# Kernel optimization log

Hardware: AMD Instinct MI355X
Metric: run time of the kernel (lower is better)

The kernel has to match this reference:

```python
import jax, jax.numpy as jnp
import numpy as np

B, S = 4096, 256
D = 32  # output_size // 4


def setup_inputs() -> dict:
    key = jax.random.key(0)
    ks = jax.random.split(key, 32)
    # continuous features
    cont_p = jax.random.normal(ks[0], (B, S, 3), dtype=jnp.float32)
    cont_c = jax.random.normal(ks[1], (B, S, 2), dtype=jnp.float32)
    # categorical features, per-column vocab sizes from Embedding tables
    vocabs_p = [2, 2, 2, 11, 34]
    cat_p = jnp.stack([
        jax.random.randint(ks[2 + i], (B, S), 0, v, dtype=jnp.int32)
        for i, v in enumerate(vocabs_p)], axis=2)
    vocabs_c = [19, 31]
    cat_c = jnp.stack([
        jax.random.randint(ks[7 + i], (B, S), 0, v, dtype=jnp.int32)
        for i, v in enumerate(vocabs_c)], axis=2)
    lengths = jax.random.randint(ks[9], (B,), 1, S + 1, dtype=jnp.int32)

    def lin(k, fan_in, fan_out):
        bound = 1.0 / np.sqrt(fan_in)
        kw, kb = jax.random.split(k)
        w = jax.random.uniform(kw, (fan_in, fan_out), jnp.float32, -bound, bound)
        b = jax.random.uniform(kb, (fan_out,), jnp.float32, -bound, bound)
        return w, b

    w_p1, b_p1 = lin(ks[10], 3, D)
    w_p2, b_p2 = lin(ks[11], D, D)
    w_c1, b_c1 = lin(ks[12], 2, D)
    w_c2, b_c2 = lin(ks[13], D, D)
    emb_gender = jax.random.normal(ks[14], (2, D), dtype=jnp.float32)
    emb_korean = jax.random.normal(ks[15], (2, D), dtype=jnp.float32)
    emb_primary = jax.random.normal(ks[16], (2, D), dtype=jnp.float32)
    emb_job = jax.random.normal(ks[17], (11, D), dtype=jnp.float32)
    emb_rep = jax.random.normal(ks[18], (34, D), dtype=jnp.float32)
    emb_place = jax.random.normal(ks[19], (19, D), dtype=jnp.float32)
    emb_add = jax.random.normal(ks[20], (31, D), dtype=jnp.float32)
    w_fc1, b_fc1 = lin(ks[21], 128, 64)
    w_fc2, b_fc2 = lin(ks[22], 64, 2)

    return dict(cont_p=cont_p, cont_c=cont_c, cat_p=cat_p, cat_c=cat_c,
                lengths=lengths,
                w_p1=w_p1, b_p1=b_p1, w_p2=w_p2, b_p2=b_p2,
                w_c1=w_c1, b_c1=b_c1, w_c2=w_c2, b_c2=b_c2,
                emb_gender=emb_gender, emb_korean=emb_korean,
                emb_primary=emb_primary, emb_job=emb_job, emb_rep=emb_rep,
                emb_place=emb_place, emb_add=emb_add,
                w_fc1=w_fc1, b_fc1=b_fc1, w_fc2=w_fc2, b_fc2=b_fc2)


def reference(cont_p, cont_c, cat_p, cat_c, lengths,
              w_p1, b_p1, w_p2, b_p2, w_c1, b_c1, w_c2, b_c2,
              emb_gender, emb_korean, emb_primary, emb_job, emb_rep,
              emb_place, emb_add, w_fc1, b_fc1, w_fc2, b_fc2):
    # small per-token MLPs on continuous features -> [B,S,D]
    hp = jax.nn.relu(cont_p @ w_p1 + b_p1) @ w_p2 + b_p2
    hc = jax.nn.relu(cont_c @ w_c1 + b_c1) @ w_c2 + b_c2
    # multi-table embedding lookups, averaged per group -> [B,S,D]
    ep = (emb_gender[cat_p[:, :, 0]] + emb_korean[cat_p[:, :, 1]] +
          emb_primary[cat_p[:, :, 2]] + emb_job[cat_p[:, :, 3]] +
          emb_rep[cat_p[:, :, 4]]) / 5.0
    ec = (emb_place[cat_c[:, :, 0]] + emb_add[cat_c[:, :, 1]]) / 2.0
    # concat order matches torch: (cat_p, cat_c, cont_p, cont_c) -> [B,S,128]
    x = jnp.concatenate([ep, ec, hp, hc], axis=2)
    # ragged mean pool over first lengths[i] positions (masked segment mean)
    mask = (jnp.arange(x.shape[1])[None, :] < lengths[:, None])
    pooled = jnp.sum(x * mask[:, :, None], axis=1) / lengths[:, None].astype(x.dtype)
    # head: relu(fc1) -> relu(fc2); dropout p=0.0 is identity
    h = jax.nn.relu(pooled @ w_fc1 + b_fc1)
    return jax.nn.relu(h @ w_fc2 + b_fc2)
```

## Files before the change

kernel.cpp:

```cpp
#include <hip/hip_runtime.h>


#define BDIM 64

__global__ __launch_bounds__(BDIM)
void mlpreg_kernel(const float* __restrict__ cont_p,
                   const float* __restrict__ cont_c,
                   const int* __restrict__ cat_p,
                   const int* __restrict__ cat_c,
                   const int* __restrict__ lengths,
                   const float* __restrict__ w_p1, const float* __restrict__ b_p1,
                   const float* __restrict__ w_p2, const float* __restrict__ b_p2,
                   const float* __restrict__ w_c1, const float* __restrict__ b_c1,
                   const float* __restrict__ w_c2, const float* __restrict__ b_c2,
                   const float* __restrict__ emb_g,  const float* __restrict__ emb_k,
                   const float* __restrict__ emb_pr, const float* __restrict__ emb_j,
                   const float* __restrict__ emb_r,  const float* __restrict__ emb_pl,
                   const float* __restrict__ emb_a,
                   const float* __restrict__ w_fc1, const float* __restrict__ b_fc1,
                   const float* __restrict__ w_fc2, const float* __restrict__ b_fc2,
                   float* __restrict__ out)
{
    constexpr int S = 256;
    __shared__ float sP4[S * 4];
    __shared__ float sC2[S * 2];
    __shared__ int   hist[96];
    __shared__ float sPacc[64];
    __shared__ float sPooled[128];

    const int lane = threadIdx.x;
    const int b    = blockIdx.x;
    int L = lengths[b];
    if (L < 1) L = 1;
    if (L > S) L = S;
    const float invL = 1.0f / (float)L;
    const float Lf   = (float)L;

    const int*   kp = cat_p  + (size_t)b * (S * 5);
    const int*   kc = cat_c  + (size_t)b * (S * 2);
    const float* gp = cont_p + (size_t)b * (S * 3);
    const float* gc = cont_c + (size_t)b * (S * 2);

    hist[lane] = 0;
    if (lane < 32) hist[64 + lane] = 0;
    __syncthreads();

    for (int t = lane; t < L; t += BDIM) {
        float c0 = gp[t * 3 + 0], c1 = gp[t * 3 + 1], c2 = gp[t * 3 + 2];
        float4 v; v.x = c0; v.y = c1; v.z = c2; v.w = 0.f;
        *(float4*)&sP4[t * 4] = v;
        float2 u = *(const float2*)(gc + t * 2);
        *(float2*)&sC2[t * 2] = u;
    }

    int sg = 0, sk = 0, spr = 0;
    for (int i = lane; i < 5 * L; i += BDIM) {
        int v = kp[i];
        int col = i % 5;
        if      (col == 0) sg  += v;
        else if (col == 1) sk  += v;
        else if (col == 2) spr += v;
        else if (col == 3) atomicAdd(&hist[v], 1);
        else               atomicAdd(&hist[11 + v], 1);
    }
    for (int i = lane; i < 2 * L; i += BDIM) {
        int v = kc[i];
        atomicAdd(&hist[(i & 1) ? (64 + v) : (45 + v)], 1);
    }
    #pragma unroll
    for (int d = 32; d; d >>= 1) {
        sg  += __shfl_xor(sg,  d);
        sk  += __shfl_xor(sk,  d);
        spr += __shfl_xor(spr, d);
    }
    __syncthreads();

    const int pr = lane >> 5, ch = lane & 31;
    const float wp0 = w_p1[ch], wp1 = w_p1[32 + ch], wp2 = w_p1[64 + ch], bp = b_p1[ch];
    const float wc0 = w_c1[ch], wc1 = w_c1[32 + ch], bc = b_c1[ch];

    float accP = 0.f, accC = 0.f;
    #pragma unroll 4
    for (int t = pr; t < L; t += 2) {
        float4 cp = *(const float4*)&sP4[t * 4];
        float2 cc = *(const float2*)&sC2[t * 2];
        accP += fmaxf(fmaf(cp.x, wp0, fmaf(cp.y, wp1, fmaf(cp.z, wp2, bp))), 0.f);
        accC += fmaxf(fmaf(cc.x, wc0, fmaf(cc.y, wc1, bc)), 0.f);
    }
    accP += __shfl_down(accP, 32);
    accC += __shfl_down(accC, 32);
    if (lane < 32) {
        sPacc[ch]      = accP * invL;
        sPacc[32 + ch] = accC * invL;
    }

    if (pr == 0) {
        float cg = (float)sg, ck = (float)sk, cp = (float)spr;
        float s0 = fmaf(Lf - cg, emb_g[ch],  fmaf(cg, emb_g[32 + ch],
                   fmaf(Lf - ck, emb_k[ch],  ck * emb_k[32 + ch])));
        float s1 = fmaf(Lf - cp, emb_pr[ch], cp * emb_pr[32 + ch]);
        #pragma unroll
        for (int r = 0; r < 11; ++r) s0 = fmaf((float)hist[r],      emb_j[r * 32 + ch], s0);
        #pragma unroll
        for (int r = 0; r < 34; r += 2) {
            s0 = fmaf((float)hist[11 + r],     emb_r[(r + 0) * 32 + ch], s0);
            s1 = fmaf((float)hist[11 + r + 1], emb_r[(r + 1) * 32 + ch], s1);
        }
        sPooled[ch] = (s0 + s1) * (invL * 0.2f);
    } else {
        float s0 = 0.f, s1 = 0.f;
        #pragma unroll
        for (int r = 0; r < 19; ++r) s0 = fmaf((float)hist[45 + r], emb_pl[r * 32 + ch], s0);
        #pragma unroll
        for (int r = 0; r < 31; r += 2) {
            s0 = fmaf((float)hist[64 + r], emb_a[(r + 0) * 32 + ch], s0);
            if (r + 1 < 31)
                s1 = fmaf((float)hist[64 + r + 1], emb_a[(r + 1) * 32 + ch], s1);
        }
        sPooled[32 + ch] = (s0 + s1) * (invL * 0.5f);
    }
    __syncthreads();

    if (pr == 0) {
        float v0 = b_p2[ch], v1 = 0.f;
        #pragma unroll
        for (int k = 0; k < 32; k += 2) {
            v0 = fmaf(sPacc[k],     w_p2[(k + 0) * 32 + ch], v0);
            v1 = fmaf(sPacc[k + 1], w_p2[(k + 1) * 32 + ch], v1);
        }
        sPooled[64 + ch] = v0 + v1;
    } else {
        float v0 = b_c2[ch], v1 = 0.f;
        #pragma unroll
        for (int k = 0; k < 32; k += 2) {
            v0 = fmaf(sPacc[32 + k],     w_c2[(k + 0) * 32 + ch], v0);
            v1 = fmaf(sPacc[32 + k + 1], w_c2[(k + 1) * 32 + ch], v1);
        }
        sPooled[96 + ch] = v0 + v1;
    }
    __syncthreads();

    const float* wk = w_fc1 + lane;
    float v0 = b_fc1[lane], v1 = 0.f, v2 = 0.f, v3 = 0.f;
    #pragma unroll 8
    for (int k = 0; k < 128; k += 4) {
        float4 x = *(const float4*)&sPooled[k];
        v0 = fmaf(x.x, wk[(size_t)(k + 0) * 64], v0);
        v1 = fmaf(x.y, wk[(size_t)(k + 1) * 64], v1);
        v2 = fmaf(x.z, wk[(size_t)(k + 2) * 64], v2);
        v3 = fmaf(x.w, wk[(size_t)(k + 3) * 64], v3);
    }
    float h = fmaxf((v0 + v1) + (v2 + v3), 0.f);

    float p0 = h * w_fc2[lane * 2 + 0];
    float p1 = h * w_fc2[lane * 2 + 1];
    #pragma unroll
    for (int d = 32; d; d >>= 1) {
        p0 += __shfl_xor(p0, d);
        p1 += __shfl_xor(p1, d);
    }
    if (lane == 0) {
        float2 o;
        o.x = fmaxf(p0 + b_fc2[0], 0.f);
        o.y = fmaxf(p1 + b_fc2[1], 0.f);
        *(float2*)&out[(size_t)b * 2] = o;
    }
}

extern "C" void kernel_launch(void* const* d_in, const int* in_sizes, int n_in,
                              void* d_out, int out_size, void* d_ws, size_t ws_size,
                              hipStream_t stream) {
    const float* cont_p = (const float*)d_in[0];
    const float* cont_c = (const float*)d_in[1];
    const int*   cat_p  = (const int*)d_in[2];
    const int*   cat_c  = (const int*)d_in[3];
    const int*   lens   = (const int*)d_in[4];
    const float* w_p1   = (const float*)d_in[5];
    const float* b_p1   = (const float*)d_in[6];
    const float* w_p2   = (const float*)d_in[7];
    const float* b_p2   = (const float*)d_in[8];
    const float* w_c1   = (const float*)d_in[9];
    const float* b_c1   = (const float*)d_in[10];
    const float* w_c2   = (const float*)d_in[11];
    const float* b_c2   = (const float*)d_in[12];
    const float* emb_g  = (const float*)d_in[13];
    const float* emb_k  = (const float*)d_in[14];
    const float* emb_pr = (const float*)d_in[15];
    const float* emb_j  = (const float*)d_in[16];
    const float* emb_r  = (const float*)d_in[17];
    const float* emb_pl = (const float*)d_in[18];
    const float* emb_a  = (const float*)d_in[19];
    const float* w_fc1  = (const float*)d_in[20];
    const float* b_fc1  = (const float*)d_in[21];
    const float* w_fc2  = (const float*)d_in[22];
    const float* b_fc2  = (const float*)d_in[23];
    float* out = (float*)d_out;

    const int B = 4096;
    hipLaunchKernelGGL(mlpreg_kernel, dim3(B), dim3(BDIM), 0, stream,
                       cont_p, cont_c, cat_p, cat_c, lens,
                       w_p1, b_p1, w_p2, b_p2, w_c1, b_c1, w_c2, b_c2,
                       emb_g, emb_k, emb_pr, emb_j, emb_r, emb_pl, emb_a,
                       w_fc1, b_fc1, w_fc2, b_fc2, out);
}
```

Baseline: 144.9 us.

## Widen per-row block to 256 threads and split all phases across four waves

Raises the block from one wave to four waves per batch row. All row inputs are loaded up front into registers with coalesced flat indexing before the shared-memory writes, so each thread has many loads in flight. The token MLP, embedding histogram dot products, second-layer MLPs and fc1 are then partitioned across waves, with cross-wave reductions through shared memory. This aims to hide global load latency and shorten the serial per-row chain, at the cost of more barriers and more threads idle in the later small phases.

```diff
diff --git a/kernel.cpp b/kernel.cpp
--- a/kernel.cpp
+++ b/kernel.cpp
@@ -1,9 +1,9 @@
 #include <hip/hip_runtime.h>
 
 
-#define BDIM 64
-
-__global__ __launch_bounds__(BDIM)
+#define BDIM 256
+
+__global__ __launch_bounds__(BDIM, 8)
 void mlpreg_kernel(const float* __restrict__ cont_p,
                    const float* __restrict__ cont_c,
                    const int* __restrict__ cat_p,
@@ -22,14 +22,17 @@
                    float* __restrict__ out)
 {
     constexpr int S = 256;
-    __shared__ float sP4[S * 4];
-    __shared__ float sC2[S * 2];
+    __shared__ float sContP[S * 3];
+    __shared__ float sContC[S * 2];
     __shared__ int   hist[96];
+    __shared__ int   sBin[4][3];
+    __shared__ float sRedP[128], sRedC[128];
     __shared__ float sPacc[64];
     __shared__ float sPooled[128];
-
-    const int lane = threadIdx.x;
-    const int b    = blockIdx.x;
+    __shared__ float sRedF[BDIM];
+
+    const int tid = threadIdx.x;
+    const int b   = blockIdx.x;
     int L = lengths[b];
     if (L < 1) L = 1;
     if (L > S) L = S;
@@ -41,129 +44,167 @@
     const float* gp = cont_p + (size_t)b * (S * 3);
     const float* gc = cont_c + (size_t)b * (S * 2);
 
-    hist[lane] = 0;
-    if (lane < 32) hist[64 + lane] = 0;
-    __syncthreads();
-
-    for (int t = lane; t < L; t += BDIM) {
-        float c0 = gp[t * 3 + 0], c1 = gp[t * 3 + 1], c2 = gp[t * 3 + 2];
-        float4 v; v.x = c0; v.y = c1; v.z = c2; v.w = 0.f;
-        *(float4*)&sP4[t * 4] = v;
-        float2 u = *(const float2*)(gc + t * 2);
-        *(float2*)&sC2[t * 2] = u;
-    }
+    const int n3 = 3 * L, n2 = 2 * L, n5 = 5 * L;
+    float rp0 = (tid       < n3) ? gp[tid]       : 0.f;
+    float rp1 = (tid + 256 < n3) ? gp[tid + 256] : 0.f;
+    float rp2 = (tid + 512 < n3) ? gp[tid + 512] : 0.f;
+    float rc0 = (tid       < n2) ? gc[tid]       : 0.f;
+    float rc1 = (tid + 256 < n2) ? gc[tid + 256] : 0.f;
+    int rk[5];
+    #pragma unroll
+    for (int j = 0; j < 5; ++j) {
+        int ii = tid + 256 * j;
+        rk[j] = (ii < n5) ? kp[ii] : -1;
+    }
+    int rq0 = (tid       < n2) ? kc[tid]       : -1;
+    int rq1 = (tid + 256 < n2) ? kc[tid + 256] : -1;
+
+    if (tid < 96) hist[tid] = 0;
+    __syncthreads();
+
+    if (tid       < n3) sContP[tid]       = rp0;
+    if (tid + 256 < n3) sContP[tid + 256] = rp1;
+    if (tid + 512 < n3) sContP[tid + 512] = rp2;
+    if (tid       < n2) sContC[tid]       = rc0;
+    if (tid + 256 < n2) sContC[tid + 256] = rc1;
 
     int sg = 0, sk = 0, spr = 0;
-    for (int i = lane; i < 5 * L; i += BDIM) {
-        int v = kp[i];
-        int col = i % 5;
-        if      (col == 0) sg  += v;
-        else if (col == 1) sk  += v;
-        else if (col == 2) spr += v;
-        else if (col == 3) atomicAdd(&hist[v], 1);
-        else               atomicAdd(&hist[11 + v], 1);
-    }
-    for (int i = lane; i < 2 * L; i += BDIM) {
-        int v = kc[i];
-        atomicAdd(&hist[(i & 1) ? (64 + v) : (45 + v)], 1);
-    }
+    #pragma unroll
+    for (int j = 0; j < 5; ++j) {
+        int ii = tid + 256 * j;
+        if (ii < n5) {
+            int col = ii % 5, v = rk[j];
+            if      (col == 0) sg  += v;
+            else if (col == 1) sk  += v;
+            else if (col == 2) spr += v;
+            else if (col == 3) atomicAdd(&hist[v], 1);
+            else               atomicAdd(&hist[11 + v], 1);
+        }
+    }
+    if (rq0 >= 0) atomicAdd(&hist[((tid & 1) ? 64 : 45) + rq0], 1);
+    if (rq1 >= 0) atomicAdd(&hist[((tid & 1) ? 64 : 45) + rq1], 1);
+
     #pragma unroll
     for (int d = 32; d; d >>= 1) {
         sg  += __shfl_xor(sg,  d);
         sk  += __shfl_xor(sk,  d);
         spr += __shfl_xor(spr, d);
     }
-    __syncthreads();
-
-    const int pr = lane >> 5, ch = lane & 31;
+    const int wv = tid >> 6, lane = tid & 63;
+    if (lane == 0) { sBin[wv][0] = sg; sBin[wv][1] = sk; sBin[wv][2] = spr; }
+    __syncthreads();
+
+    const int g8 = tid >> 5, ch = tid & 31, h = lane >> 5;
     const float wp0 = w_p1[ch], wp1 = w_p1[32 + ch], wp2 = w_p1[64 + ch], bp = b_p1[ch];
     const float wc0 = w_c1[ch], wc1 = w_c1[32 + ch], bc = b_c1[ch];
-
     float accP = 0.f, accC = 0.f;
-    #pragma unroll 4
-    for (int t = pr; t < L; t += 2) {
-        float4 cp = *(const float4*)&sP4[t * 4];
-        float2 cc = *(const float2*)&sC2[t * 2];
-        accP += fmaxf(fmaf(cp.x, wp0, fmaf(cp.y, wp1, fmaf(cp.z, wp2, bp))), 0.f);
-        accC += fmaxf(fmaf(cc.x, wc0, fmaf(cc.y, wc1, bc)), 0.f);
+    #pragma unroll 2
+    for (int t = g8; t < L; t += 8) {
+        float c0 = sContP[3 * t], c1 = sContP[3 * t + 1], c2 = sContP[3 * t + 2];
+        float d0 = sContC[2 * t], d1 = sContC[2 * t + 1];
+        accP += fmaxf(fmaf(c0, wp0, fmaf(c1, wp1, fmaf(c2, wp2, bp))), 0.f);
+        accC += fmaxf(fmaf(d0, wc0, fmaf(d1, wc1, bc)), 0.f);
     }
     accP += __shfl_down(accP, 32);
     accC += __shfl_down(accC, 32);
-    if (lane < 32) {
-        sPacc[ch]      = accP * invL;
-        sPacc[32 + ch] = accC * invL;
-    }
-
-    if (pr == 0) {
-        float cg = (float)sg, ck = (float)sk, cp = (float)spr;
-        float s0 = fmaf(Lf - cg, emb_g[ch],  fmaf(cg, emb_g[32 + ch],
-                   fmaf(Lf - ck, emb_k[ch],  ck * emb_k[32 + ch])));
-        float s1 = fmaf(Lf - cp, emb_pr[ch], cp * emb_pr[32 + ch]);
-        #pragma unroll
-        for (int r = 0; r < 11; ++r) s0 = fmaf((float)hist[r],      emb_j[r * 32 + ch], s0);
-        #pragma unroll
-        for (int r = 0; r < 34; r += 2) {
-            s0 = fmaf((float)hist[11 + r],     emb_r[(r + 0) * 32 + ch], s0);
-            s1 = fmaf((float)hist[11 + r + 1], emb_r[(r + 1) * 32 + ch], s1);
-        }
-        sPooled[ch] = (s0 + s1) * (invL * 0.2f);
+    if (lane < 32) { sRedP[wv * 32 + ch] = accP; sRedC[wv * 32 + ch] = accC; }
+    __syncthreads();
+
+    if (wv == 0) {
+        float sgT  = (float)(sBin[0][0] + sBin[1][0] + sBin[2][0] + sBin[3][0]);
+        float skT  = (float)(sBin[0][1] + sBin[1][1] + sBin[2][1] + sBin[3][1]);
+        float sprT = (float)(sBin[0][2] + sBin[1][2] + sBin[2][2] + sBin[3][2]);
+        float s = 0.f;
+        if (h == 0) {
+            s  = fmaf(Lf - sgT,  emb_g[ch],  sgT  * emb_g[32 + ch]);
+            s += fmaf(Lf - sprT, emb_pr[ch], sprT * emb_pr[32 + ch]);
+            #pragma unroll
+            for (int r = 0; r < 6; ++r)  s = fmaf((float)hist[r],      emb_j[r * 32 + ch], s);
+            #pragma unroll
+            for (int r = 0; r < 17; ++r) s = fmaf((float)hist[11 + r], emb_r[r * 32 + ch], s);
+        } else {
+            s = fmaf(Lf - skT, emb_k[ch], skT * emb_k[32 + ch]);
+            #pragma unroll
+            for (int r = 6; r < 11; ++r)  s = fmaf((float)hist[r],      emb_j[r * 32 + ch], s);
+            #pragma unroll
+            for (int r = 17; r < 34; ++r) s = fmaf((float)hist[11 + r], emb_r[r * 32 + ch], s);
+        }
+        s += __shfl_down(s, 32);
+        if (h == 0) sPooled[ch] = s * (invL * 0.2f);
+    } else if (wv == 1) {
+        float s = 0.f;
+        if (h == 0) {
+            #pragma unroll
+            for (int r = 0; r < 10; ++r) s = fmaf((float)hist[45 + r], emb_pl[r * 32 + ch], s);
+            #pragma unroll
+            for (int r = 0; r < 16; ++r) s = fmaf((float)hist[64 + r], emb_a[r * 32 + ch], s);
+        } else {
+            #pragma unroll
+            for (int r = 10; r < 19; ++r) s = fmaf((float)hist[45 + r], emb_pl[r * 32 + ch], s);
+            #pragma unroll
+            for (int r = 16; r < 31; ++r) s = fmaf((float)hist[64 + r], emb_a[r * 32 + ch], s);
+        }
+        s += __shfl_down(s, 32);
+        if (h == 0) sPooled[32 + ch] = s * (invL * 0.5f);
+    } else if (wv == 2) {
+        if (lane < 32)
+            sPacc[ch] = (sRedP[ch] + sRedP[32 + ch] + sRedP[64 + ch] + sRedP[96 + ch]) * invL;
     } else {
-        float s0 = 0.f, s1 = 0.f;
-        #pragma unroll
-        for (int r = 0; r < 19; ++r) s0 = fmaf((float)hist[45 + r], emb_pl[r * 32 + ch], s0);
-        #pragma unroll
-        for (int r = 0; r < 31; r += 2) {
-            s0 = fmaf((float)hist[64 + r], emb_a[(r + 0) * 32 + ch], s0);
-            if (r + 1 < 31)
-                s1 = fmaf((float)hist[64 + r + 1], emb_a[(r + 1) * 32 + ch], s1);
-        }
-        sPooled[32 + ch] = (s0 + s1) * (invL * 0.5f);
-    }
-    __syncthreads();
-
-    if (pr == 0) {
-        float v0 = b_p2[ch], v1 = 0.f;
-        #pragma unroll
-        for (int k = 0; k < 32; k += 2) {
-            v0 = fmaf(sPacc[k],     w_p2[(k + 0) * 32 + ch], v0);
-            v1 = fmaf(sPacc[k + 1], w_p2[(k + 1) * 32 + ch], v1);
-        }
-        sPooled[64 + ch] = v0 + v1;
-    } else {
-        float v0 = b_c2[ch], v1 = 0.f;
-        #pragma unroll
-        for (int k = 0; k < 32; k += 2) {
-            v0 = fmaf(sPacc[32 + k],     w_c2[(k + 0) * 32 + ch], v0);
-            v1 = fmaf(sPacc[32 + k + 1], w_c2[(k + 1) * 32 + ch], v1);
-        }
-        sPooled[96 + ch] = v0 + v1;
-    }
-    __syncthreads();
-
-    const float* wk = w_fc1 + lane;
-    float v0 = b_fc1[lane], v1 = 0.f, v2 = 0.f, v3 = 0.f;
-    #pragma unroll 8
-    for (int k = 0; k < 128; k += 4) {
-        float4 x = *(const float4*)&sPooled[k];
-        v0 = fmaf(x.x, wk[(size_t)(k + 0) * 64], v0);
-        v1 = fmaf(x.y, wk[(size_t)(k + 1) * 64], v1);
-        v2 = fmaf(x.z, wk[(size_t)(k + 2) * 64], v2);
-        v3 = fmaf(x.w, wk[(size_t)(k + 3) * 64], v3);
-    }
-    float h = fmaxf((v0 + v1) + (v2 + v3), 0.f);
-
-    float p0 = h * w_fc2[lane * 2 + 0];
-    float p1 = h * w_fc2[lane * 2 + 1];
-    #pragma unroll
-    for (int d = 32; d; d >>= 1) {
-        p0 += __shfl_xor(p0, d);
-        p1 += __shfl_xor(p1, d);
-    }
-    if (lane == 0) {
-        float2 o;
-        o.x = fmaxf(p0 + b_fc2[0], 0.f);
-        o.y = fmaxf(p1 + b_fc2[1], 0.f);
-        *(float2*)&out[(size_t)b * 2] = o;
+        if (lane < 32)
+            sPacc[32 + ch] = (sRedC[ch] + sRedC[32 + ch] + sRedC[64 + ch] + sRedC[96 + ch]) * invL;
+    }
+    __syncthreads();
+
+    if (wv == 2) {
+        const int kb = h * 16;
+        float v = (h == 0) ? b_p2[ch] : 0.f;
+        #pragma unroll
+        for (int k = 0; k < 16; ++k) v = fmaf(sPacc[kb + k], w_p2[(kb + k) * 32 + ch], v);
+        v += __shfl_down(v, 32);
+        if (h == 0) sPooled[64 + ch] = v;
+    } else if (wv == 3) {
+        const int kb = h * 16;
+        float v = (h == 0) ? b_c2[ch] : 0.f;
+        #pragma unroll
+        for (int k = 0; k < 16; ++k) v = fmaf(sPacc[32 + kb + k], w_c2[(kb + k) * 32 + ch], v);
+        v += __shfl_down(v, 32);
+        if (h == 0) sPooled[96 + ch] = v;
+    }
+    __syncthreads();
+
+    {
+        const int o = tid & 63, part = tid >> 6;
+        const float* wk = w_fc1 + (size_t)(part * 32) * 64 + o;
+        const float* xk = sPooled + part * 32;
+        float v0 = 0.f, v1 = 0.f, v2 = 0.f, v3 = 0.f;
+        #pragma unroll
+        for (int k = 0; k < 32; k += 4) {
+            v0 = fmaf(xk[k + 0], wk[(size_t)(k + 0) * 64], v0);
+            v1 = fmaf(xk[k + 1], wk[(size_t)(k + 1) * 64], v1);
+            v2 = fmaf(xk[k + 2], wk[(size_t)(k + 2) * 64], v2);
+            v3 = fmaf(xk[k + 3], wk[(size_t)(k + 3) * 64], v3);
+        }
+        sRedF[tid] = (v0 + v1) + (v2 + v3);
+    }
+    __syncthreads();
+
+    if (wv == 0) {
+        float hv = b_fc1[lane] + (sRedF[lane] + sRedF[64 + lane])
+                               + (sRedF[128 + lane] + sRedF[192 + lane]);
+        hv = fmaxf(hv, 0.f);
+        float p0 = hv * w_fc2[lane * 2 + 0];
+        float p1 = hv * w_fc2[lane * 2 + 1];
+        #pragma unroll
+        for (int d = 32; d; d >>= 1) {
+            p0 += __shfl_xor(p0, d);
+            p1 += __shfl_xor(p1, d);
+        }
+        if (lane == 0) {
+            float2 o2;
+            o2.x = fmaxf(p0 + b_fc2[0], 0.f);
+            o2.y = fmaxf(p1 + b_fc2[1], 0.f);
+            *(float2*)&out[(size_t)b * 2] = o2;
+        }
     }
 }
 
```

Result: slower. 148.8 us (+2.7%).

## Split into per-task pooling kernel and batched head kernel via workspace

Applied to the files above, without the earlier changes.

The single fused kernel is split in two. The first kernel launches three blocks per batch row, one each for the categorical histogram, the cont_p MLP pool and the cont_c MLP pool, and writes partial results to the workspace. The second kernel processes 8 rows per 256-thread block, stages the embedding tables in shared memory, and batches the embedding matmul, second-layer projections and the FC head. This spreads the per-row latency across more blocks and reuses weights across rows, at the cost of an extra launch and a workspace round trip.

```diff
diff --git a/kernel.cpp b/kernel.cpp
--- a/kernel.cpp
+++ b/kernel.cpp
@@ -1,169 +1,193 @@
 #include <hip/hip_runtime.h>
 
 
-#define BDIM 64
-
-__global__ __launch_bounds__(BDIM)
-void mlpreg_kernel(const float* __restrict__ cont_p,
-                   const float* __restrict__ cont_c,
-                   const int* __restrict__ cat_p,
-                   const int* __restrict__ cat_c,
-                   const int* __restrict__ lengths,
-                   const float* __restrict__ w_p1, const float* __restrict__ b_p1,
-                   const float* __restrict__ w_p2, const float* __restrict__ b_p2,
-                   const float* __restrict__ w_c1, const float* __restrict__ b_c1,
-                   const float* __restrict__ w_c2, const float* __restrict__ b_c2,
-                   const float* __restrict__ emb_g,  const float* __restrict__ emb_k,
-                   const float* __restrict__ emb_pr, const float* __restrict__ emb_j,
-                   const float* __restrict__ emb_r,  const float* __restrict__ emb_pl,
-                   const float* __restrict__ emb_a,
-                   const float* __restrict__ w_fc1, const float* __restrict__ b_fc1,
-                   const float* __restrict__ w_fc2, const float* __restrict__ b_fc2,
-                   float* __restrict__ out)
+#define WS_PACC_OFF 0
+#define WS_HIST_OFF (4096 * 64)
+
+__global__ __launch_bounds__(64)
+void mlpreg_pool(const float* __restrict__ cont_p,
+                 const float* __restrict__ cont_c,
+                 const int* __restrict__ cat_p,
+                 const int* __restrict__ cat_c,
+                 const int* __restrict__ lengths,
+                 const float* __restrict__ w_p1, const float* __restrict__ b_p1,
+                 const float* __restrict__ w_c1, const float* __restrict__ b_c1,
+                 float* __restrict__ ws)
 {
     constexpr int S = 256;
-    __shared__ float sP4[S * 4];
-    __shared__ float sC2[S * 2];
-    __shared__ int   hist[96];
-    __shared__ float sPacc[64];
-    __shared__ float sPooled[128];
-
+    __shared__ float sT[S * 3];
+    __shared__ int   h[96];
+
+    const int bx   = blockIdx.x;
+    const int task = bx % 3;
+    const int b    = bx / 3;
     const int lane = threadIdx.x;
-    const int b    = blockIdx.x;
+
     int L = lengths[b];
-    if (L < 1) L = 1;
-    if (L > S) L = S;
+    L = (L < 1) ? 1 : (L > S ? S : L);
     const float invL = 1.0f / (float)L;
-    const float Lf   = (float)L;
-
-    const int*   kp = cat_p  + (size_t)b * (S * 5);
-    const int*   kc = cat_c  + (size_t)b * (S * 2);
-    const float* gp = cont_p + (size_t)b * (S * 3);
-    const float* gc = cont_c + (size_t)b * (S * 2);
-
-    hist[lane] = 0;
-    if (lane < 32) hist[64 + lane] = 0;
+
+    if (task == 0) {
+        h[lane] = 0;
+        if (lane + 64 < 96) h[lane + 64] = 0;
+        __syncthreads();
+        const int* kp = cat_p + (size_t)b * (S * 5);
+        const int* kc = cat_c + (size_t)b * (S * 2);
+        int sg = 0, sk = 0, spr = 0;
+        for (int i = lane; i < 5 * L; i += 64) {
+            int v = kp[i], col = i % 5;
+            if      (col == 0) sg  += v;
+            else if (col == 1) sk  += v;
+            else if (col == 2) spr += v;
+            else if (col == 3) atomicAdd(&h[v], 1);
+            else               atomicAdd(&h[11 + v], 1);
+        }
+        for (int i = lane; i < 2 * L; i += 64) {
+            int v = kc[i];
+            atomicAdd(&h[(i & 1) ? (64 + v) : (45 + v)], 1);
+        }
+        #pragma unroll
+        for (int d = 32; d; d >>= 1) {
+            sg  += __shfl_xor(sg,  d);
+            sk  += __shfl_xor(sk,  d);
+            spr += __shfl_xor(spr, d);
+        }
+        __syncthreads();
+        float* o = ws + WS_HIST_OFF + (size_t)b * 104;
+        for (int i = lane; i < 95; i += 64) o[i] = (float)h[i];
+        if (lane == 0) {
+            o[95] = (float)sg; o[96] = (float)sk; o[97] = (float)spr;
+            o[98] = (float)L;
+        }
+    } else if (task == 1) {
+        const float* gp = cont_p + (size_t)b * (S * 3);
+        for (int i = lane; i < 3 * L; i += 64) sT[i] = gp[i];
+        const int ch = lane & 31, pr = lane >> 5;
+        const float w0 = w_p1[ch], w1 = w_p1[32 + ch], w2 = w_p1[64 + ch],
+                    bb = b_p1[ch];
+        __syncthreads();
+        float acc = 0.f;
+        #pragma unroll 4
+        for (int t = pr; t < L; t += 2) {
+            float c0 = sT[3 * t], c1 = sT[3 * t + 1], c2 = sT[3 * t + 2];
+            acc += fmaxf(fmaf(c0, w0, fmaf(c1, w1, fmaf(c2, w2, bb))), 0.f);
+        }
+        acc += __shfl_down(acc, 32);
+        if (lane < 32) ws[WS_PACC_OFF + (size_t)b * 64 + ch] = acc * invL;
+    } else {
+        const float* gc = cont_c + (size_t)b * (S * 2);
+        for (int i = lane; i < 2 * L; i += 64) sT[i] = gc[i];
+        const int ch = lane & 31, pr = lane >> 5;
+        const float w0 = w_c1[ch], w1 = w_c1[32 + ch], bb = b_c1[ch];
+        __syncthreads();
+        float acc = 0.f;
+        #pragma unroll 4
+        for (int t = pr; t < L; t += 2) {
+            float d0 = sT[2 * t], d1 = sT[2 * t + 1];
+            acc += fmaxf(fmaf(d0, w0, fmaf(d1, w1, bb)), 0.f);
+        }
+        acc += __shfl_down(acc, 32);
+        if (lane < 32) ws[WS_PACC_OFF + (size_t)b * 64 + 32 + ch] = acc * invL;
+    }
+}
+
+__global__ __launch_bounds__(256)
+void mlpreg_head(const float* __restrict__ emb_g,  const float* __restrict__ emb_k,
+                 const float* __restrict__ emb_pr, const float* __restrict__ emb_j,
+                 const float* __restrict__ emb_r,  const float* __restrict__ emb_pl,
+                 const float* __restrict__ emb_a,
+                 const float* __restrict__ w_p2, const float* __restrict__ b_p2,
+                 const float* __restrict__ w_c2, const float* __restrict__ b_c2,
+                 const float* __restrict__ w_fc1, const float* __restrict__ b_fc1,
+                 const float* __restrict__ w_fc2, const float* __restrict__ b_fc2,
+                 const float* __restrict__ ws, float* __restrict__ out)
+{
+    __shared__ float T[101 * 32];
+    __shared__ float hF[8][104];
+    __shared__ float pacc[8][64];
+    __shared__ float sPool[8][128];
+    __shared__ float sH[8][64];
+
+    const int tid   = threadIdx.x;
+    const int rbase = blockIdx.x * 8;
+
+    for (int i = tid; i < 11 * 32; i += 256) T[i]           = emb_j[i];
+    for (int i = tid; i < 34 * 32; i += 256) T[11 * 32 + i] = emb_r[i];
+    for (int i = tid; i < 19 * 32; i += 256) T[45 * 32 + i] = emb_pl[i];
+    for (int i = tid; i < 31 * 32; i += 256) T[64 * 32 + i] = emb_a[i];
+    for (int i = tid; i < 2 * 32;  i += 256) T[95 * 32 + i] = emb_g[i];
+    for (int i = tid; i < 2 * 32;  i += 256) T[97 * 32 + i] = emb_k[i];
+    for (int i = tid; i < 2 * 32;  i += 256) T[99 * 32 + i] = emb_pr[i];
+    for (int i = tid; i < 8 * 104; i += 256)
+        hF[i / 104][i % 104] = ws[WS_HIST_OFF + (size_t)(rbase + i / 104) * 104 + (i % 104)];
+    for (int i = tid; i < 8 * 64; i += 256)
+        pacc[i / 64][i % 64] = ws[WS_PACC_OFF + (size_t)(rbase + i / 64) * 64 + (i % 64)];
     __syncthreads();
 
-    for (int t = lane; t < L; t += BDIM) {
-        float c0 = gp[t * 3 + 0], c1 = gp[t * 3 + 1], c2 = gp[t * 3 + 2];
-        float4 v; v.x = c0; v.y = c1; v.z = c2; v.w = 0.f;
-        *(float4*)&sP4[t * 4] = v;
-        float2 u = *(const float2*)(gc + t * 2);
-        *(float2*)&sC2[t * 2] = u;
-    }
-
-    int sg = 0, sk = 0, spr = 0;
-    for (int i = lane; i < 5 * L; i += BDIM) {
-        int v = kp[i];
-        int col = i % 5;
-        if      (col == 0) sg  += v;
-        else if (col == 1) sk  += v;
-        else if (col == 2) spr += v;
-        else if (col == 3) atomicAdd(&hist[v], 1);
-        else               atomicAdd(&hist[11 + v], 1);
-    }
-    for (int i = lane; i < 2 * L; i += BDIM) {
-        int v = kc[i];
-        atomicAdd(&hist[(i & 1) ? (64 + v) : (45 + v)], 1);
-    }
-    #pragma unroll
-    for (int d = 32; d; d >>= 1) {
-        sg  += __shfl_xor(sg,  d);
-        sk  += __shfl_xor(sk,  d);
-        spr += __shfl_xor(spr, d);
+    const int rr = tid >> 5, ch = tid & 31;
+    {
+        const float Lf = hF[rr][98], invL = 1.0f / Lf;
+        const float sg = hF[rr][95], sk = hF[rr][96], spr = hF[rr][97];
+        float sep = fmaf(Lf - sg,  T[95 * 32 + ch], sg  * T[96 * 32 + ch])
+                  + fmaf(Lf - sk,  T[97 * 32 + ch], sk  * T[98 * 32 + ch])
+                  + fmaf(Lf - spr, T[99 * 32 + ch], spr * T[100 * 32 + ch]);
+        float sec = 0.f;
+        #pragma unroll
+        for (int r = 0; r < 45; ++r)  sep = fmaf(hF[rr][r], T[r * 32 + ch], sep);
+        #pragma unroll
+        for (int r = 45; r < 95; ++r) sec = fmaf(hF[rr][r], T[r * 32 + ch], sec);
+        sPool[rr][ch]      = sep * (invL * 0.2f);
+        sPool[rr][32 + ch] = sec * (invL * 0.5f);
+
+        float wp[32], wc[32];
+        #pragma unroll
+        for (int k = 0; k < 32; ++k) wp[k] = w_p2[k * 32 + ch];
+        #pragma unroll
+        for (int k = 0; k < 32; ++k) wc[k] = w_c2[k * 32 + ch];
+        float vp = b_p2[ch], vc = b_c2[ch];
+        #pragma unroll
+        for (int k = 0; k < 32; ++k) {
+            vp = fmaf(pacc[rr][k],      wp[k], vp);
+            vc = fmaf(pacc[rr][32 + k], wc[k], vc);
+        }
+        sPool[rr][64 + ch] = vp;
+        sPool[rr][96 + ch] = vc;
     }
     __syncthreads();
 
-    const int pr = lane >> 5, ch = lane & 31;
-    const float wp0 = w_p1[ch], wp1 = w_p1[32 + ch], wp2 = w_p1[64 + ch], bp = b_p1[ch];
-    const float wc0 = w_c1[ch], wc1 = w_c1[32 + ch], bc = b_c1[ch];
-
-    float accP = 0.f, accC = 0.f;
-    #pragma unroll 4
-    for (int t = pr; t < L; t += 2) {
-        float4 cp = *(const float4*)&sP4[t * 4];
-        float2 cc = *(const float2*)&sC2[t * 2];
-        accP += fmaxf(fmaf(cp.x, wp0, fmaf(cp.y, wp1, fmaf(cp.z, wp2, bp))), 0.f);
-        accC += fmaxf(fmaf(cc.x, wc0, fmaf(cc.y, wc1, bc)), 0.f);
-    }
-    accP += __shfl_down(accP, 32);
-    accC += __shfl_down(accC, 32);
-    if (lane < 32) {
-        sPacc[ch]      = accP * invL;
-        sPacc[32 + ch] = accC * invL;
-    }
-
-    if (pr == 0) {
-        float cg = (float)sg, ck = (float)sk, cp = (float)spr;
-        float s0 = fmaf(Lf - cg, emb_g[ch],  fmaf(cg, emb_g[32 + ch],
-                   fmaf(Lf - ck, emb_k[ch],  ck * emb_k[32 + ch])));
-        float s1 = fmaf(Lf - cp, emb_pr[ch], cp * emb_pr[32 + ch]);
-        #pragma unroll
-        for (int r = 0; r < 11; ++r) s0 = fmaf((float)hist[r],      emb_j[r * 32 + ch], s0);
-        #pragma unroll
-        for (int r = 0; r < 34; r += 2) {
-            s0 = fmaf((float)hist[11 + r],     emb_r[(r + 0) * 32 + ch], s0);
-            s1 = fmaf((float)hist[11 + r + 1], emb_r[(r + 1) * 32 + ch], s1);
-        }
-        sPooled[ch] = (s0 + s1) * (invL * 0.2f);
-    } else {
-        float s0 = 0.f, s1 = 0.f;
-        #pragma unroll
-        for (int r = 0; r < 19; ++r) s0 = fmaf((float)hist[45 + r], emb_pl[r * 32 + ch], s0);
-        #pragma unroll
-        for (int r = 0; r < 31; r += 2) {
-            s0 = fmaf((float)hist[64 + r], emb_a[(r + 0) * 32 + ch], s0);
-            if (r + 1 < 31)
-                s1 = fmaf((float)hist[64 + r + 1], emb_a[(r + 1) * 32 + ch], s1);
-        }
-        sPooled[32 + ch] = (s0 + s1) * (invL * 0.5f);
+    {
+        const int o = tid & 63, rq = tid >> 6;
+        float x0 = 0.f, x1 = 0.f, y0 = 0.f, y1 = 0.f;
+        #pragma unroll 8
+        for (int k = 0; k < 128; k += 2) {
+            float wa = w_fc1[(size_t)(k + 0) * 64 + o];
+            float wb = w_fc1[(size_t)(k + 1) * 64 + o];
+            x0 = fmaf(sPool[rq][k],         wa, x0);
+            x1 = fmaf(sPool[rq][k + 1],     wb, x1);
+            y0 = fmaf(sPool[rq + 4][k],     wa, y0);
+            y1 = fmaf(sPool[rq + 4][k + 1], wb, y1);
+        }
+        const float bo = b_fc1[o];
+        sH[rq][o]     = fmaxf(bo + x0 + x1, 0.f);
+        sH[rq + 4][o] = fmaxf(bo + y0 + y1, 0.f);
     }
     __syncthreads();
 
-    if (pr == 0) {
-        float v0 = b_p2[ch], v1 = 0.f;
-        #pragma unroll
-        for (int k = 0; k < 32; k += 2) {
-            v0 = fmaf(sPacc[k],     w_p2[(k + 0) * 32 + ch], v0);
-            v1 = fmaf(sPacc[k + 1], w_p2[(k + 1) * 32 + ch], v1);
-        }
-        sPooled[64 + ch] = v0 + v1;
-    } else {
-        float v0 = b_c2[ch], v1 = 0.f;
-        #pragma unroll
-        for (int k = 0; k < 32; k += 2) {
-            v0 = fmaf(sPacc[32 + k],     w_c2[(k + 0) * 32 + ch], v0);
-            v1 = fmaf(sPacc[32 + k + 1], w_c2[(k + 1) * 32 + ch], v1);
-        }
-        sPooled[96 + ch] = v0 + v1;
-    }
-    __syncthreads();
-
-    const float* wk = w_fc1 + lane;
-    float v0 = b_fc1[lane], v1 = 0.f, v2 = 0.f, v3 = 0.f;
-    #pragma unroll 8
-    for (int k = 0; k < 128; k += 4) {
-        float4 x = *(const float4*)&sPooled[k];
-        v0 = fmaf(x.x, wk[(size_t)(k + 0) * 64], v0);
-        v1 = fmaf(x.y, wk[(size_t)(k + 1) * 64], v1);
-        v2 = fmaf(x.z, wk[(size_t)(k + 2) * 64], v2);
-        v3 = fmaf(x.w, wk[(size_t)(k + 3) * 64], v3);
-    }
-    float h = fmaxf((v0 + v1) + (v2 + v3), 0.f);
-
-    float p0 = h * w_fc2[lane * 2 + 0];
-    float p1 = h * w_fc2[lane * 2 + 1];
-    #pragma unroll
-    for (int d = 32; d; d >>= 1) {
-        p0 += __shfl_xor(p0, d);
-        p1 += __shfl_xor(p1, d);
-    }
-    if (lane == 0) {
-        float2 o;
-        o.x = fmaxf(p0 + b_fc2[0], 0.f);
-        o.y = fmaxf(p1 + b_fc2[1], 0.f);
-        *(float2*)&out[(size_t)b * 2] = o;
+    {
+        float h0 = sH[rr][ch], h1 = sH[rr][32 + ch];
+        float p0 = fmaf(h0, w_fc2[ch * 2 + 0], h1 * w_fc2[(32 + ch) * 2 + 0]);
+        float p1 = fmaf(h0, w_fc2[ch * 2 + 1], h1 * w_fc2[(32 + ch) * 2 + 1]);
+        #pragma unroll
+        for (int d = 16; d; d >>= 1) {
+            p0 += __shfl_xor(p0, d);
+            p1 += __shfl_xor(p1, d);
+        }
+        if (ch == 0) {
+            float2 o2;
+            o2.x = fmaxf(p0 + b_fc2[0], 0.f);
+            o2.y = fmaxf(p1 + b_fc2[1], 0.f);
+            *(float2*)&out[(size_t)(rbase + rr) * 2] = o2;
+        }
     }
 }
 
@@ -195,11 +219,13 @@
     const float* w_fc2  = (const float*)d_in[22];
     const float* b_fc2  = (const float*)d_in[23];
     float* out = (float*)d_out;
-
-    const int B = 4096;
-    hipLaunchKernelGGL(mlpreg_kernel, dim3(B), dim3(BDIM), 0, stream,
+    float* ws  = (float*)d_ws;
+
+    hipLaunchKernelGGL(mlpreg_pool, dim3(3 * 4096), dim3(64), 0, stream,
                        cont_p, cont_c, cat_p, cat_c, lens,
-                       w_p1, b_p1, w_p2, b_p2, w_c1, b_c1, w_c2, b_c2,
+                       w_p1, b_p1, w_c1, b_c1, ws);
+    hipLaunchKernelGGL(mlpreg_head, dim3(512), dim3(256), 0, stream,
                        emb_g, emb_k, emb_pr, emb_j, emb_r, emb_pl, emb_a,
-                       w_fc1, b_fc1, w_fc2, b_fc2, out);
+                       w_p2, b_p2, w_c2, b_c2, w_fc1, b_fc1, w_fc2, b_fc2,
+                       ws, out);
 }
```

Measured after the change: 149.8 us. 1.03x slower.

## Process two batch rows per block, sharing weight loads and vectorizing input loads

Applied to the files above, without the earlier changes.

Each 64-thread block now handles two batch rows. Embedding, fc2-layer and head weights are loaded once and applied to both rows, and the continuous inputs are copied to LDS with float4 loads. The categorical loop now reads all columns of a token in one iteration instead of using modulo dispatch. Each half-wave walks one row's tokens serially for the first MLP layer. This halves the grid to 2048 blocks, which lowers parallelism, and ragged lengths can leave one half-wave idle.

```diff
diff --git a/kernel.cpp b/kernel.cpp
--- a/kernel.cpp
+++ b/kernel.cpp
@@ -22,148 +22,189 @@
                    float* __restrict__ out)
 {
     constexpr int S = 256;
-    __shared__ float sP4[S * 4];
-    __shared__ float sC2[S * 2];
-    __shared__ int   hist[96];
-    __shared__ float sPacc[64];
-    __shared__ float sPooled[128];
+    __shared__ float sP[2][S * 3];
+    __shared__ float sC[2][S * 2];
+    __shared__ int   hist[2][96];
+    __shared__ float sPacc[2][64];
+    __shared__ float sPool[2][128];
 
     const int lane = threadIdx.x;
-    const int b    = blockIdx.x;
-    int L = lengths[b];
-    if (L < 1) L = 1;
-    if (L > S) L = S;
-    const float invL = 1.0f / (float)L;
-    const float Lf   = (float)L;
-
-    const int*   kp = cat_p  + (size_t)b * (S * 5);
-    const int*   kc = cat_c  + (size_t)b * (S * 2);
-    const float* gp = cont_p + (size_t)b * (S * 3);
-    const float* gc = cont_c + (size_t)b * (S * 2);
-
-    hist[lane] = 0;
-    if (lane < 32) hist[64 + lane] = 0;
-    __syncthreads();
-
-    for (int t = lane; t < L; t += BDIM) {
-        float c0 = gp[t * 3 + 0], c1 = gp[t * 3 + 1], c2 = gp[t * 3 + 2];
-        float4 v; v.x = c0; v.y = c1; v.z = c2; v.w = 0.f;
-        *(float4*)&sP4[t * 4] = v;
-        float2 u = *(const float2*)(gc + t * 2);
-        *(float2*)&sC2[t * 2] = u;
-    }
-
-    int sg = 0, sk = 0, spr = 0;
-    for (int i = lane; i < 5 * L; i += BDIM) {
-        int v = kp[i];
-        int col = i % 5;
-        if      (col == 0) sg  += v;
-        else if (col == 1) sk  += v;
-        else if (col == 2) spr += v;
-        else if (col == 3) atomicAdd(&hist[v], 1);
-        else               atomicAdd(&hist[11 + v], 1);
-    }
-    for (int i = lane; i < 2 * L; i += BDIM) {
-        int v = kc[i];
-        atomicAdd(&hist[(i & 1) ? (64 + v) : (45 + v)], 1);
+    const int b0 = blockIdx.x * 2, b1 = b0 + 1;
+
+    int L0 = lengths[b0]; L0 = (L0 < 1) ? 1 : (L0 > S ? S : L0);
+    int L1 = lengths[b1]; L1 = (L1 < 1) ? 1 : (L1 > S ? S : L1);
+    const float L0f = (float)L0, L1f = (float)L1;
+    const float invL0 = 1.0f / L0f, invL1 = 1.0f / L1f;
+
+    { int i = lane;            ((int*)hist)[i] = 0;
+      i += 64;                 ((int*)hist)[i] = 0;
+      i += 64;                 ((int*)hist)[i] = 0; }
+
+    const int ch = lane & 31, h = lane >> 5;
+    const float wp0 = w_p1[ch], wp1 = w_p1[32 + ch], wp2 = w_p1[64 + ch], bp = b_p1[ch];
+    const float wc0 = w_c1[ch], wc1 = w_c1[32 + ch], bc = b_c1[ch];
+
+    {
+        const float4* gp0 = (const float4*)(cont_p + (size_t)b0 * (S * 3));
+        const float4* gp1 = (const float4*)(cont_p + (size_t)b1 * (S * 3));
+        const float4* gc0 = (const float4*)(cont_c + (size_t)b0 * (S * 2));
+        const float4* gc1 = (const float4*)(cont_c + (size_t)b1 * (S * 2));
+        const int n0 = (3 * L0 + 3) >> 2, n1 = (3 * L1 + 3) >> 2;
+        const int m0 = (2 * L0 + 3) >> 2, m1 = (2 * L1 + 3) >> 2;
+        for (int i = lane; i < n0; i += 64) *(float4*)&sP[0][4 * i] = gp0[i];
+        for (int i = lane; i < n1; i += 64) *(float4*)&sP[1][4 * i] = gp1[i];
+        for (int i = lane; i < m0; i += 64) *(float4*)&sC[0][4 * i] = gc0[i];
+        for (int i = lane; i < m1; i += 64) *(float4*)&sC[1][4 * i] = gc1[i];
+    }
+
+    int sg0 = 0, sk0 = 0, sp0 = 0, sg1 = 0, sk1 = 0, sp1 = 0;
+    {
+        const int*  kp0 = cat_p + (size_t)b0 * (S * 5);
+        const int*  kp1 = cat_p + (size_t)b1 * (S * 5);
+        const int2* kc0 = (const int2*)(cat_c + (size_t)b0 * (S * 2));
+        const int2* kc1 = (const int2*)(cat_c + (size_t)b1 * (S * 2));
+        #pragma unroll 2
+        for (int t = lane; t < L0; t += 64) {
+            int v0 = kp0[5 * t], v1 = kp0[5 * t + 1], v2 = kp0[5 * t + 2],
+                v3 = kp0[5 * t + 3], v4 = kp0[5 * t + 4];
+            int2 q = kc0[t];
+            sg0 += v0; sk0 += v1; sp0 += v2;
+            atomicAdd(&hist[0][v3], 1);
+            atomicAdd(&hist[0][11 + v4], 1);
+            atomicAdd(&hist[0][45 + q.x], 1);
+            atomicAdd(&hist[0][64 + q.y], 1);
+        }
+        #pragma unroll 2
+        for (int t = lane; t < L1; t += 64) {
+            int v0 = kp1[5 * t], v1 = kp1[5 * t + 1], v2 = kp1[5 * t + 2],
+                v3 = kp1[5 * t + 3], v4 = kp1[5 * t + 4];
+            int2 q = kc1[t];
+            sg1 += v0; sk1 += v1; sp1 += v2;
+            atomicAdd(&hist[1][v3], 1);
+            atomicAdd(&hist[1][11 + v4], 1);
+            atomicAdd(&hist[1][45 + q.x], 1);
+            atomicAdd(&hist[1][64 + q.y], 1);
+        }
     }
     #pragma unroll
     for (int d = 32; d; d >>= 1) {
-        sg  += __shfl_xor(sg,  d);
-        sk  += __shfl_xor(sk,  d);
-        spr += __shfl_xor(spr, d);
+        sg0 += __shfl_xor(sg0, d); sk0 += __shfl_xor(sk0, d); sp0 += __shfl_xor(sp0, d);
+        sg1 += __shfl_xor(sg1, d); sk1 += __shfl_xor(sk1, d); sp1 += __shfl_xor(sp1, d);
     }
     __syncthreads();
 
-    const int pr = lane >> 5, ch = lane & 31;
-    const float wp0 = w_p1[ch], wp1 = w_p1[32 + ch], wp2 = w_p1[64 + ch], bp = b_p1[ch];
-    const float wc0 = w_c1[ch], wc1 = w_c1[32 + ch], bc = b_c1[ch];
-
-    float accP = 0.f, accC = 0.f;
-    #pragma unroll 4
-    for (int t = pr; t < L; t += 2) {
-        float4 cp = *(const float4*)&sP4[t * 4];
-        float2 cc = *(const float2*)&sC2[t * 2];
-        accP += fmaxf(fmaf(cp.x, wp0, fmaf(cp.y, wp1, fmaf(cp.z, wp2, bp))), 0.f);
-        accC += fmaxf(fmaf(cc.x, wc0, fmaf(cc.y, wc1, bc)), 0.f);
-    }
-    accP += __shfl_down(accP, 32);
-    accC += __shfl_down(accC, 32);
-    if (lane < 32) {
-        sPacc[ch]      = accP * invL;
-        sPacc[32 + ch] = accC * invL;
-    }
-
-    if (pr == 0) {
-        float cg = (float)sg, ck = (float)sk, cp = (float)spr;
-        float s0 = fmaf(Lf - cg, emb_g[ch],  fmaf(cg, emb_g[32 + ch],
-                   fmaf(Lf - ck, emb_k[ch],  ck * emb_k[32 + ch])));
-        float s1 = fmaf(Lf - cp, emb_pr[ch], cp * emb_pr[32 + ch]);
-        #pragma unroll
-        for (int r = 0; r < 11; ++r) s0 = fmaf((float)hist[r],      emb_j[r * 32 + ch], s0);
-        #pragma unroll
-        for (int r = 0; r < 34; r += 2) {
-            s0 = fmaf((float)hist[11 + r],     emb_r[(r + 0) * 32 + ch], s0);
-            s1 = fmaf((float)hist[11 + r + 1], emb_r[(r + 1) * 32 + ch], s1);
-        }
-        sPooled[ch] = (s0 + s1) * (invL * 0.2f);
+    {
+        const int   Lr   = h ? L1 : L0;
+        const float invr = h ? invL1 : invL0;
+        const float* tp = sP[h];
+        const float* tc = sC[h];
+        float aP = 0.f, aC = 0.f;
+        #pragma unroll 4
+        for (int t = 0; t < Lr; ++t) {
+            float c0 = tp[3 * t], c1 = tp[3 * t + 1], c2 = tp[3 * t + 2];
+            float2 d2 = *(const float2*)&tc[2 * t];
+            aP += fmaxf(fmaf(c0, wp0, fmaf(c1, wp1, fmaf(c2, wp2, bp))), 0.f);
+            aC += fmaxf(fmaf(d2.x, wc0, fmaf(d2.y, wc1, bc)), 0.f);
+        }
+        sPacc[h][ch]      = aP * invr;
+        sPacc[h][32 + ch] = aC * invr;
+    }
+    __syncthreads();
+
+    if (h == 0) {
+        float g0 = emb_g[ch],  g1 = emb_g[32 + ch];
+        float k0 = emb_k[ch],  k1 = emb_k[32 + ch];
+        float p0 = emb_pr[ch], p1 = emb_pr[32 + ch];
+        float fg0 = (float)sg0, fk0 = (float)sk0, fp0 = (float)sp0;
+        float fg1 = (float)sg1, fk1 = (float)sk1, fp1 = (float)sp1;
+        float A0 = fmaf(L0f - fg0, g0, fg0 * g1) + fmaf(L0f - fk0, k0, fk0 * k1)
+                 + fmaf(L0f - fp0, p0, fp0 * p1);
+        float A1 = fmaf(L1f - fg1, g0, fg1 * g1) + fmaf(L1f - fk1, k0, fk1 * k1)
+                 + fmaf(L1f - fp1, p0, fp1 * p1);
+        #pragma unroll
+        for (int r = 0; r < 11; ++r) {
+            float w = emb_j[r * 32 + ch];
+            A0 = fmaf((float)hist[0][r], w, A0);
+            A1 = fmaf((float)hist[1][r], w, A1);
+        }
+        #pragma unroll
+        for (int r = 0; r < 34; ++r) {
+            float w = emb_r[r * 32 + ch];
+            A0 = fmaf((float)hist[0][11 + r], w, A0);
+            A1 = fmaf((float)hist[1][11 + r], w, A1);
+        }
+        sPool[0][ch] = A0 * (invL0 * 0.2f);
+        sPool[1][ch] = A1 * (invL1 * 0.2f);
+
+        float v0 = b_p2[ch], v1 = v0;
+        #pragma unroll
+        for (int k = 0; k < 32; ++k) {
+            float w = w_p2[k * 32 + ch];
+            v0 = fmaf(sPacc[0][k], w, v0);
+            v1 = fmaf(sPacc[1][k], w, v1);
+        }
+        sPool[0][64 + ch] = v0;
+        sPool[1][64 + ch] = v1;
     } else {
-        float s0 = 0.f, s1 = 0.f;
-        #pragma unroll
-        for (int r = 0; r < 19; ++r) s0 = fmaf((float)hist[45 + r], emb_pl[r * 32 + ch], s0);
-        #pragma unroll
-        for (int r = 0; r < 31; r += 2) {
-            s0 = fmaf((float)hist[64 + r], emb_a[(r + 0) * 32 + ch], s0);
-            if (r + 1 < 31)
-                s1 = fmaf((float)hist[64 + r + 1], emb_a[(r + 1) * 32 + ch], s1);
-        }
-        sPooled[32 + ch] = (s0 + s1) * (invL * 0.5f);
+        float A0 = 0.f, A1 = 0.f;
+        #pragma unroll
+        for (int r = 0; r < 19; ++r) {
+            float w = emb_pl[r * 32 + ch];
+            A0 = fmaf((float)hist[0][45 + r], w, A0);
+            A1 = fmaf((float)hist[1][45 + r], w, A1);
+        }
+        #pragma unroll
+        for (int r = 0; r < 31; ++r) {
+            float w = emb_a[r * 32 + ch];
+            A0 = fmaf((float)hist[0][64 + r], w, A0);
+            A1 = fmaf((float)hist[1][64 + r], w, A1);
+        }
+        sPool[0][32 + ch] = A0 * (invL0 * 0.5f);
+        sPool[1][32 + ch] = A1 * (invL1 * 0.5f);
+
+        float v0 = b_c2[ch], v1 = v0;
+        #pragma unroll
+        for (int k = 0; k < 32; ++k) {
+            float w = w_c2[k * 32 + ch];
+            v0 = fmaf(sPacc[0][32 + k], w, v0);
+            v1 = fmaf(sPacc[1][32 + k], w, v1);
+        }
+        sPool[0][96 + ch] = v0;
+        sPool[1][96 + ch] = v1;
     }
     __syncthreads();
 
-    if (pr == 0) {
-        float v0 = b_p2[ch], v1 = 0.f;
-        #pragma unroll
-        for (int k = 0; k < 32; k += 2) {
-            v0 = fmaf(sPacc[k],     w_p2[(k + 0) * 32 + ch], v0);
-            v1 = fmaf(sPacc[k + 1], w_p2[(k + 1) * 32 + ch], v1);
-        }
-        sPooled[64 + ch] = v0 + v1;
-    } else {
-        float v0 = b_c2[ch], v1 = 0.f;
-        #pragma unroll
-        for (int k = 0; k < 32; k += 2) {
-            v0 = fmaf(sPacc[32 + k],     w_c2[(k + 0) * 32 + ch], v0);
-            v1 = fmaf(sPacc[32 + k + 1], w_c2[(k + 1) * 32 + ch], v1);
-        }
-        sPooled[96 + ch] = v0 + v1;
-    }
-    __syncthreads();
-
-    const float* wk = w_fc1 + lane;
-    float v0 = b_fc1[lane], v1 = 0.f, v2 = 0.f, v3 = 0.f;
-    #pragma unroll 8
-    for (int k = 0; k < 128; k += 4) {
-        float4 x = *(const float4*)&sPooled[k];
-        v0 = fmaf(x.x, wk[(size_t)(k + 0) * 64], v0);
-        v1 = fmaf(x.y, wk[(size_t)(k + 1) * 64], v1);
-        v2 = fmaf(x.z, wk[(size_t)(k + 2) * 64], v2);
-        v3 = fmaf(x.w, wk[(size_t)(k + 3) * 64], v3);
-    }
-    float h = fmaxf((v0 + v1) + (v2 + v3), 0.f);
-
-    float p0 = h * w_fc2[lane * 2 + 0];
-    float p1 = h * w_fc2[lane * 2 + 1];
-    #pragma unroll
-    for (int d = 32; d; d >>= 1) {
-        p0 += __shfl_xor(p0, d);
-        p1 += __shfl_xor(p1, d);
-    }
-    if (lane == 0) {
-        float2 o;
-        o.x = fmaxf(p0 + b_fc2[0], 0.f);
-        o.y = fmaxf(p1 + b_fc2[1], 0.f);
-        *(float2*)&out[(size_t)b * 2] = o;
+    {
+        const int o = lane;
+        float x0 = b_fc1[o], y0 = 0.f;
+        float x1 = x0,       y1 = 0.f;
+        #pragma unroll 8
+        for (int k = 0; k < 128; k += 2) {
+            float wa = w_fc1[(size_t)k * 64 + o];
+            float wb = w_fc1[(size_t)(k + 1) * 64 + o];
+            float u0 = sPool[0][k], u1 = sPool[0][k + 1];
+            float s0 = sPool[1][k], s1 = sPool[1][k + 1];
+            x0 = fmaf(u0, wa, x0); y0 = fmaf(u1, wb, y0);
+            x1 = fmaf(s0, wa, x1); y1 = fmaf(s1, wb, y1);
+        }
+        float h0 = fmaxf(x0 + y0, 0.f);
+        float h1 = fmaxf(x1 + y1, 0.f);
+        float wa = w_fc2[2 * o], wb = w_fc2[2 * o + 1];
+        float q00 = h0 * wa, q01 = h0 * wb, q10 = h1 * wa, q11 = h1 * wb;
+        #pragma unroll
+        for (int d = 32; d; d >>= 1) {
+            q00 += __shfl_xor(q00, d); q01 += __shfl_xor(q01, d);
+            q10 += __shfl_xor(q10, d); q11 += __shfl_xor(q11, d);
+        }
+        if (lane == 0) {
+            float bb0 = b_fc2[0], bb1 = b_fc2[1];
+            float4 o4;
+            o4.x = fmaxf(q00 + bb0, 0.f);
+            o4.y = fmaxf(q01 + bb1, 0.f);
+            o4.z = fmaxf(q10 + bb0, 0.f);
+            o4.w = fmaxf(q11 + bb1, 0.f);
+            *(float4*)&out[(size_t)b0 * 2] = o4;
+        }
     }
 }
 
@@ -196,8 +237,7 @@
     const float* b_fc2  = (const float*)d_in[23];
     float* out = (float*)d_out;
 
-    const int B = 4096;
-    hipLaunchKernelGGL(mlpreg_kernel, dim3(B), dim3(BDIM), 0, stream,
+    hipLaunchKernelGGL(mlpreg_kernel, dim3(2048), dim3(BDIM), 0, stream,
                        cont_p, cont_c, cat_p, cat_c, lens,
                        w_p1, b_p1, w_p2, b_p2, w_c1, b_c1, w_c2, b_c2,
                        emb_g, emb_k, emb_pr, emb_j, emb_r, emb_pl, emb_a,
```

Result: faster. 139.9 us (-3.5%).
